# Kernel optimization log

Measured on AMD Instinct MI355X. Metric: run time of the kernel, lower is better.

Reference implementation:

```python
import jax, jax.numpy as jnp
import numpy as np

NUM_HEADS = 16


def setup_inputs() -> dict:
    key = jax.random.key(0)
    ks = jax.random.split(key, 9)
    B, S, D = 2, 2048, 2048
    s = 1.0 / np.sqrt(D)
    return {
        "x": jax.random.normal(ks[0], (B, S, D), jnp.float32),
        "Wq": jax.random.normal(ks[1], (D, D), jnp.float32) * s,
        "bq": jax.random.normal(ks[2], (D,), jnp.float32) * 0.01,
        "Wk": jax.random.normal(ks[3], (D, D), jnp.float32) * s,
        "bk": jax.random.normal(ks[4], (D,), jnp.float32) * 0.01,
        "Wv": jax.random.normal(ks[5], (D, D), jnp.float32) * s,
        "bv": jax.random.normal(ks[6], (D,), jnp.float32) * 0.01,
        "Wo": jax.random.normal(ks[7], (D, D), jnp.float32) * s,
        "bo": jax.random.normal(ks[8], (D,), jnp.float32) * 0.01,
    }


def reference(x, Wq, bq, Wk, bk, Wv, bv, Wo, bo):
    B, S, D = x.shape
    H = NUM_HEADS
    dh = D // H
    # torch Linear: y = x @ W.T + b
    def proj(W, b):
        return (x @ W.T + b).reshape(B, S, H, dh).transpose(0, 2, 1, 3)  # [B,H,S,dh]
    Q = proj(Wq, bq)
    K = proj(Wk, bk)
    V = proj(Wv, bv)
    scores = jnp.einsum('bhqd,bhkd->bhqk', Q, K) / jnp.sqrt(jnp.float32(dh))
    causal = jnp.tril(jnp.ones((S, S), dtype=bool))  # allow k <= q
    scores = jnp.where(causal, scores, -jnp.inf)
    attn = jax.nn.softmax(scores, axis=-1)
    out = jnp.einsum('bhqk,bhkd->bhqd', attn, V)
    out = out.transpose(0, 2, 1, 3).reshape(B, S, D)
    return out @ Wo.T + bo
```

## Files before the change

### kernel.cpp

```cpp
#include <hip/hip_runtime.h>
#include <hip/hip_bf16.h>

#define B_  2
#define S_  2048
#define D_  2048
#define H_  16
#define DH_ 128
#define M_  (B_*S_)

typedef __hip_bfloat16 bf16;
typedef float v4f __attribute__((ext_vector_type(4)));
typedef short v8s __attribute__((ext_vector_type(8)));

__device__ __forceinline__ short f2s(float x) {
  bf16 h = __float2bfloat16(x);
  return *reinterpret_cast<const short*>(&h);
}
__device__ __forceinline__ v8s ld8(const float* p) {
  v4f a = *reinterpret_cast<const v4f*>(p);
  v4f b = *reinterpret_cast<const v4f*>(p + 4);
  v8s r = { f2s(a[0]), f2s(a[1]), f2s(a[2]), f2s(a[3]),
            f2s(b[0]), f2s(b[1]), f2s(b[2]), f2s(b[3]) };
  return r;
}
__device__ __forceinline__ void store_out(bf16* p, float v)  { *p = __float2bfloat16(v); }
__device__ __forceinline__ void store_out(float* p, float v) { *p = v; }

__device__ __forceinline__ void gll16(const bf16* g, bf16* l) {
  __builtin_amdgcn_global_load_lds((const __attribute__((address_space(1))) void*)g,
                                   (__attribute__((address_space(3))) void*)l,
                                   16, 0, 0);
}

__global__ __launch_bounds__(256) void cvt_f32_bf16(const float* __restrict__ in,
                                                    bf16* __restrict__ out, int n8) {
  int i = blockIdx.x * 256 + threadIdx.x;
  if (i >= n8) return;
  *reinterpret_cast<v8s*>(out + (size_t)i * 8) = ld8(in + (size_t)i * 8);
}

__global__ __launch_bounds__(256) void cvt3_f32_bf16(const float* __restrict__ a, bf16* __restrict__ oa,
                                                     const float* __restrict__ b, bf16* __restrict__ ob,
                                                     const float* __restrict__ c, bf16* __restrict__ oc) {
  const int bx = blockIdx.x;
  if (bx < 4096) {
    size_t i = (size_t)bx * 256 + threadIdx.x;
    *reinterpret_cast<v8s*>(oa + i * 8) = ld8(a + i * 8);
  } else if (bx < 6144) {
    size_t i = (size_t)(bx - 4096) * 256 + threadIdx.x;
    *reinterpret_cast<v8s*>(ob + i * 8) = ld8(b + i * 8);
  } else {
    size_t i = (size_t)(bx - 6144) * 256 + threadIdx.x;
    *reinterpret_cast<v8s*>(oc + i * 8) = ld8(c + i * 8);
  }
}

template <int PR>
__device__ __forceinline__ void stage_pair(const bf16* Arow, const bf16* Wrow,
                                           int ktile, bf16* AsD, bf16* BsD,
                                           int tid, int wave) {
  const int k0 = ktile * 64;
#pragma unroll
  for (int u = 0; u < 2; ++u) {
    const int i = PR * 2 + u;
    const int blk = i * 512 + tid;
    if (i < 4) {
      const int row = blk >> 3, c = blk & 7;
      gll16(Arow + (size_t)row * D_ + k0 + ((c ^ (row & 7)) << 3),
            AsD + (i * 512 + wave * 64) * 8);
    } else {
      const int bb = blk - 2048;
      const int row = bb >> 3, c = bb & 7;
      gll16(Wrow + (size_t)row * D_ + k0 + ((c ^ (row & 7)) << 3),
            BsD + ((i - 4) * 512 + wave * 64) * 8);
    }
  }
}

__global__ __launch_bounds__(512, 2) void gemm_qk8(const bf16* __restrict__ A,
                                                   const bf16* __restrict__ W,
                                                   const float* __restrict__ bias0,
                                                   const float* __restrict__ bias1,
                                                   bf16* __restrict__ out0,
                                                   bf16* __restrict__ out1) {
  __shared__ __align__(16) bf16 As0[256 * 64];
  __shared__ __align__(16) bf16 Bs0[256 * 64];
  __shared__ __align__(16) bf16 As1[256 * 64];
  __shared__ __align__(16) bf16 Bs1[256 * 64];
  const int tid  = threadIdx.x;
  const int lane = tid & 63, wave = tid >> 6;
  const int wm = wave >> 2, wn = wave & 3;
  const int quad = lane >> 4, l16 = lane & 15;
  const int swz  = l16 & 7;
  const int bm = blockIdx.y * 256, bn = blockIdx.x * 256;
  const bf16* Arow = A + (size_t)bm * D_;
  const bf16* Wrow = W + (size_t)bn * D_;

  v4f acc[8][4] = {};

  stage_pair<0>(Arow, Wrow, 0, As0, Bs0, tid, wave);
  stage_pair<1>(Arow, Wrow, 0, As0, Bs0, tid, wave);
  stage_pair<2>(Arow, Wrow, 0, As0, Bs0, tid, wave);
  stage_pair<3>(Arow, Wrow, 0, As0, Bs0, tid, wave);

  constexpr int NITER = (D_ / 64) / 2;
  for (int j = 0; j < NITER; ++j) {
    const bool notlast = (j + 1 < NITER);
#pragma unroll
    for (int p = 0; p < 8; ++p) {
      const bf16* Ard = (p < 4) ? As0 : As1;
      const bf16* Brd = (p < 4) ? Bs0 : Bs1;
      bf16* AsD = (p < 4) ? As1 : As0;
      bf16* BsD = (p < 4) ? Bs1 : Bs0;
      const int tstage = (p < 4) ? (2 * j + 1) : (2 * j + 2);

      if (p == 0) {
        stage_pair<0>(Arow, Wrow, tstage, AsD, BsD, tid, wave);
        asm volatile("s_waitcnt vmcnt(2)" ::: "memory");
        __builtin_amdgcn_sched_barrier(0);
        __builtin_amdgcn_s_barrier();
        __builtin_amdgcn_sched_barrier(0);
      } else if (p == 4) {
        if (notlast) {
          stage_pair<0>(Arow, Wrow, tstage, AsD, BsD, tid, wave);
          asm volatile("s_waitcnt vmcnt(2)" ::: "memory");
        } else {
          asm volatile("s_waitcnt vmcnt(0)" ::: "memory");
        }
        __builtin_amdgcn_sched_barrier(0);
        __builtin_amdgcn_s_barrier();
        __builtin_amdgcn_sched_barrier(0);
      } else if (p < 4) {
        if (p == 1) stage_pair<1>(Arow, Wrow, tstage, AsD, BsD, tid, wave);
        if (p == 2) stage_pair<2>(Arow, Wrow, tstage, AsD, BsD, tid, wave);
        if (p == 3) stage_pair<3>(Arow, Wrow, tstage, AsD, BsD, tid, wave);
      } else {
        if (notlast) {
          if (p == 5) stage_pair<1>(Arow, Wrow, tstage, AsD, BsD, tid, wave);
          if (p == 6) stage_pair<2>(Arow, Wrow, tstage, AsD, BsD, tid, wave);
          if (p == 7) stage_pair<3>(Arow, Wrow, tstage, AsD, BsD, tid, wave);
        }
      }

      const int pp = p & 3;
      v8s af[2][2], bfr[4][2];
#pragma unroll
      for (int mi = 0; mi < 2; ++mi)
#pragma unroll
        for (int kk = 0; kk < 2; ++kk) {
          const int row = wm * 128 + (pp * 2 + mi) * 16 + l16;
          af[mi][kk] = *reinterpret_cast<const v8s*>(
              &Ard[row * 64 + (((kk * 4 + quad) ^ swz) << 3)]);
        }
#pragma unroll
      for (int ni = 0; ni < 4; ++ni)
#pragma unroll
        for (int kk = 0; kk < 2; ++kk) {
          const int row = wn * 64 + ni * 16 + l16;
          bfr[ni][kk] = *reinterpret_cast<const v8s*>(
              &Brd[row * 64 + (((kk * 4 + quad) ^ swz) << 3)]);
        }
      __builtin_amdgcn_s_setprio(1);
#pragma unroll
      for (int kk = 0; kk < 2; ++kk)
#pragma unroll
        for (int mi = 0; mi < 2; ++mi)
#pragma unroll
          for (int ni = 0; ni < 4; ++ni)
            acc[pp * 2 + mi][ni] = __builtin_amdgcn_mfma_f32_16x16x32_bf16(
                af[mi][kk], bfr[ni][kk], acc[pp * 2 + mi][ni], 0, 0, 0);
      __builtin_amdgcn_s_setprio(0);
      __builtin_amdgcn_s_barrier();
      __builtin_amdgcn_sched_barrier(0);
    }
  }

  constexpr float QSCALE = 0.12752003912f;
  const int proj = bn >> 11;
  const float* bias = proj ? bias1 : bias0;
  bf16* outp = proj ? out1 : out0;
  const int bnl = bn & 2047;
#pragma unroll
  for (int ni = 0; ni < 4; ++ni) {
    const int nl = bnl + wn * 64 + ni * 16 + l16;
    const float bv = bias[nl];
    const int hh = nl >> 7, d = nl & (DH_ - 1);
#pragma unroll
    for (int mi = 0; mi < 8; ++mi) {
      const int m0 = bm + wm * 128 + mi * 16 + quad * 4;
#pragma unroll
      for (int r = 0; r < 4; ++r) {
        const int m = m0 + r;
        float v = acc[mi][ni][r] + bv;
        if (!proj) v *= QSCALE;
        const int bb = m >> 11, s = m & (S_ - 1);
        outp[((size_t)(bb * H_ + hh) * S_ + s) * DH_ + d] = __float2bfloat16(v);
      }
    }
  }
}

template <int MODE, typename TOUT>
__global__ __launch_bounds__(256) void gemm_bt(const bf16* __restrict__ A,
                                               const bf16* __restrict__ W,
                                               const float* __restrict__ bias0,
                                               TOUT* __restrict__ out0) {
  __shared__ __align__(16) bf16 As[128 * 64];
  __shared__ __align__(16) bf16 Bs[128 * 64];
  const int tid  = threadIdx.x;
  const int lane = tid & 63, wave = tid >> 6;
  const int wm = wave >> 1, wn = wave & 1;
  const int quad = lane >> 4, l16 = lane & 15;
  const int swz  = l16 & 7;
  const int bm = blockIdx.y * 128, bn = blockIdx.x * 128;

  const bf16* Arow = A + (size_t)bm * D_;
  const bf16* Wrow = W + (size_t)bn * D_;

  v4f acc[4][4] = {};
  for (int k0 = 0; k0 < D_; k0 += 64) {
#pragma unroll
    for (int j = 0; j < 4; ++j) {
      const int blk = j * 256 + tid;
      const int row = blk >> 3, c = blk & 7;
      const int gcol = k0 + (((c ^ (row & 7)) << 3));
      gll16(Arow + (size_t)row * D_ + gcol, As + j * 2048 + wave * 512);
      gll16(Wrow + (size_t)row * D_ + gcol, Bs + j * 2048 + wave * 512);
    }
    __syncthreads();
    v8s af[4][2], bfr[4][2];
#pragma unroll
    for (int mi = 0; mi < 4; ++mi)
#pragma unroll
      for (int kk = 0; kk < 2; ++kk)
        af[mi][kk] = *reinterpret_cast<const v8s*>(
            &As[(wm * 64 + mi * 16 + l16) * 64 + (((kk * 4 + quad) ^ swz) << 3)]);
#pragma unroll
    for (int ni = 0; ni < 4; ++ni)
#pragma unroll
      for (int kk = 0; kk < 2; ++kk)
        bfr[ni][kk] = *reinterpret_cast<const v8s*>(
            &Bs[(wn * 64 + ni * 16 + l16) * 64 + (((kk * 4 + quad) ^ swz) << 3)]);
#pragma unroll
    for (int kk = 0; kk < 2; ++kk)
#pragma unroll
      for (int mi = 0; mi < 4; ++mi)
#pragma unroll
        for (int ni = 0; ni < 4; ++ni)
          acc[mi][ni] = __builtin_amdgcn_mfma_f32_16x16x32_bf16(
              af[mi][kk], bfr[ni][kk], acc[mi][ni], 0, 0, 0);
    __syncthreads();
  }

#pragma unroll
  for (int ni = 0; ni < 4; ++ni) {
    const int nl = bn + wn * 64 + ni * 16 + l16;
    const float bv = bias0[nl];
#pragma unroll
    for (int mi = 0; mi < 4; ++mi) {
      const int m0 = bm + wm * 64 + mi * 16 + quad * 4;
#pragma unroll
      for (int r = 0; r < 4; ++r) {
        const int m = m0 + r;
        float v = acc[mi][ni][r] + bv;
        size_t idx;
        if (MODE == 2) {
          int b = m >> 11, s = m & (S_ - 1);
          int h = nl >> 7, d = nl & (DH_ - 1);
          idx = ((size_t)(b * H_ + h) * DH_ + d) * S_ + s;
        } else {
          idx = (size_t)m * D_ + nl;
        }
        store_out(out0 + idx, v);
      }
    }
  }
}

#define QBLK 128
__global__ __launch_bounds__(512, 4) void attn_fused(const bf16* __restrict__ Q,
                                                     const bf16* __restrict__ K,
                                                     const bf16* __restrict__ Vt,
                                                     bf16* __restrict__ Oa) {
  __shared__ __align__(16) bf16 Ks[64 * 128];
  __shared__ __align__(16) bf16 Vs[128 * 64];
  __shared__ __align__(16) bf16 Ps[8][16 * 72];
  const int tid  = threadIdx.x;
  const int lane = tid & 63, wave = tid >> 6;
  const int quad = lane >> 4, l16 = lane & 15;
  const int swz  = l16 & 7;
  const int qtd = (int)gridDim.x - 1 - (int)blockIdx.x;
  const int qt  = (blockIdx.y & 16) ? (int)blockIdx.x : qtd;
  const int bh = blockIdx.y;
  const int b = bh >> 4, h = bh & 15;
  const bf16* Qh = Q  + (size_t)bh * S_ * DH_;
  const bf16* Kh = K  + (size_t)bh * S_ * DH_;
  const bf16* Vh = Vt + (size_t)bh * DH_ * S_;

  const int qrow0 = qt * QBLK + wave * 16;
  v8s qf[4];
#pragma unroll
  for (int kk = 0; kk < 4; ++kk)
    qf[kk] = *reinterpret_cast<const v8s*>(&Qh[(size_t)(qrow0 + l16) * DH_ + kk * 32 + quad * 8]);

  v4f acc_o[8] = {};
  float m_i[4], l_i[4];
#pragma unroll
  for (int r = 0; r < 4; ++r) { m_i[r] = -1.0e30f; l_i[r] = 0.f; }

  const int nkt = 2 * qt + 2;
  for (int kt = 0; kt < nkt; ++kt) {
    const int kbase = kt * 64;
#pragma unroll
    for (int rr = 0; rr < 2; ++rr) {
      const int g = rr * 512 + tid;
      const int krow = g >> 4, kc = g & 15;
      gll16(Kh + (size_t)(kbase + krow) * DH_ + ((kc ^ (krow & 7)) << 3),
            Ks + rr * 4096 + wave * 512);
      const int vrow = g >> 3, vc = g & 7;
      gll16(Vh + (size_t)vrow * S_ + kbase + ((vc ^ (vrow & 7)) << 3),
            Vs + rr * 4096 + wave * 512);
    }
    __syncthreads();

    const bool active = (kbase <= qrow0 + 15);
    if (active) {
      v4f sc[4];
      __builtin_amdgcn_s_setprio(1);
#pragma unroll
      for (int nt = 0; nt < 4; ++nt) {
        v4f a = {};
#pragma unroll
        for (int kk = 0; kk < 4; ++kk) {
          v8s kf = *reinterpret_cast<const v8s*>(
              &Ks[(nt * 16 + l16) * 128 + (((kk * 4 + quad) ^ swz) << 3)]);
          a = __builtin_amdgcn_mfma_f32_16x16x32_bf16(qf[kk], kf, a, 0, 0, 0);
        }
        sc[nt] = a;
      }
      __builtin_amdgcn_s_setprio(0);
      if (kbase + 63 > qrow0) {
#pragma unroll
        for (int nt = 0; nt < 4; ++nt)
#pragma unroll
          for (int r = 0; r < 4; ++r) {
            int kc2 = kbase + nt * 16 + l16;
            int qr = qrow0 + quad * 4 + r;
            if (kc2 > qr) sc[nt][r] = -1.0e30f;
          }
      }
#pragma unroll
      for (int r = 0; r < 4; ++r) {
        float mx = fmaxf(fmaxf(sc[0][r], sc[1][r]), fmaxf(sc[2][r], sc[3][r]));
        mx = fmaxf(mx, __shfl_xor(mx, 1));
        mx = fmaxf(mx, __shfl_xor(mx, 2));
        mx = fmaxf(mx, __shfl_xor(mx, 4));
        mx = fmaxf(mx, __shfl_xor(mx, 8));
        if (mx > m_i[r] + 8.0f) {
          float alpha = exp2f(m_i[r] - mx);
          m_i[r] = mx;
          l_i[r] *= alpha;
#pragma unroll
          for (int nt8 = 0; nt8 < 8; ++nt8) acc_o[nt8][r] *= alpha;
        }
        const float mm = m_i[r];
        float s0 = exp2f(sc[0][r] - mm);
        float s1 = exp2f(sc[1][r] - mm);
        float s2 = exp2f(sc[2][r] - mm);
        float s3 = exp2f(sc[3][r] - mm);
        sc[0][r] = s0; sc[1][r] = s1; sc[2][r] = s2; sc[3][r] = s3;
        float t = s0 + s1 + s2 + s3;
        t += __shfl_xor(t, 1); t += __shfl_xor(t, 2);
        t += __shfl_xor(t, 4); t += __shfl_xor(t, 8);
        l_i[r] += t;
      }
#pragma unroll
      for (int nt = 0; nt < 4; ++nt)
#pragma unroll
        for (int r = 0; r < 4; ++r)
          Ps[wave][(quad * 4 + r) * 72 + nt * 16 + l16] = __float2bfloat16(sc[nt][r]);
      asm volatile("s_waitcnt lgkmcnt(0)" ::: "memory");
      __builtin_amdgcn_s_setprio(1);
#pragma unroll
      for (int kk2 = 0; kk2 < 2; ++kk2) {
        v8s pf = *reinterpret_cast<const v8s*>(&Ps[wave][l16 * 72 + kk2 * 32 + quad * 8]);
#pragma unroll
        for (int nt8 = 0; nt8 < 8; ++nt8) {
          v8s vf = *reinterpret_cast<const v8s*>(
              &Vs[(nt8 * 16 + l16) * 64 + (((kk2 * 4 + quad) ^ swz) << 3)]);
          acc_o[nt8] = __builtin_amdgcn_mfma_f32_16x16x32_bf16(pf, vf, acc_o[nt8], 0, 0, 0);
        }
      }
      __builtin_amdgcn_s_setprio(0);
    }
    __syncthreads();
  }

#pragma unroll
  for (int r = 0; r < 4; ++r) {
    const float inv = 1.0f / l_i[r];
    const int srow = qrow0 + quad * 4 + r;
#pragma unroll
    for (int nt8 = 0; nt8 < 8; ++nt8)
      Oa[((size_t)b * S_ + srow) * D_ + h * DH_ + nt8 * 16 + l16] =
          __float2bfloat16(acc_o[nt8][r] * inv);
  }
}

extern "C" void kernel_launch(void* const* d_in, const int* in_sizes, int n_in,
                              void* d_out, int out_size, void* d_ws, size_t ws_size,
                              hipStream_t stream) {
  if (n_in != 9 ||
      in_sizes[0] != M_ * D_ ||
      in_sizes[1] != D_ * D_ || in_sizes[2] != D_ ||
      in_sizes[3] != D_ * D_ || in_sizes[4] != D_ ||
      in_sizes[5] != D_ * D_ || in_sizes[6] != D_ ||
      in_sizes[7] != D_ * D_ || in_sizes[8] != D_ ||
      out_size != M_ * D_)
    return;

  const float* x  = (const float*)d_in[0];
  const float* Wq = (const float*)d_in[1];
  const float* bq = (const float*)d_in[2];
  const float* Wk = (const float*)d_in[3];
  const float* bk = (const float*)d_in[4];
  const float* Wv = (const float*)d_in[5];
  const float* bv = (const float*)d_in[6];
  const float* Wo = (const float*)d_in[7];
  const float* bo = (const float*)d_in[8];
  float* out = (float*)d_out;

  const size_t NT = (size_t)M_ * D_;
  const size_t WN = (size_t)D_ * D_;
  bf16* qws   = (bf16*)d_out;
  bf16* xbf   = (bf16*)d_out + NT;
  bf16* kws   = (bf16*)d_ws;
  bf16* vtw   = kws + NT;
  bf16* aws   = vtw + NT;
  bf16* wqk   = aws;
  bf16* wv_s  = aws;
  bf16* wo_s  = kws;

  const int N8W = D_ * D_ / 8;

  dim3 bb(256);
  cvt3_f32_bf16<<<8192, bb, 0, stream>>>(x, xbf, Wq, wqk, Wk, wqk + WN);

  gemm_qk8<<<dim3(16, 16), dim3(512), 0, stream>>>(xbf, wqk, bq, bk, qws, kws);

  cvt_f32_bf16<<<N8W / 256, bb, 0, stream>>>(Wv, wv_s, N8W);
  gemm_bt<2, bf16><<<dim3(16, 32), bb, 0, stream>>>(xbf, wv_s, bv, vtw);

  attn_fused<<<dim3(S_ / QBLK, B_ * H_), dim3(512), 0, stream>>>(qws, kws, vtw, aws);

  cvt_f32_bf16<<<N8W / 256, bb, 0, stream>>>(Wo, wo_s, N8W);
  gemm_bt<3, float><<<dim3(16, 32), bb, 0, stream>>>(aws, wo_s, bo, out);
}
```

Baseline: 407.1 us.

## Restructure QK GEMM main loop with register double-buffered A fragments

Rewrites the QK projection GEMM K-loop so each k-tile loads its B fragments once rather than re-reading them for every quarter. A fragments are ping-ponged across two register sets so LDS reads for the next quarter overlap the MFMAs of the current one. Global stages for the next tile are interleaved between MFMA groups, and the per-quarter barriers are replaced by two barriers per k-tile. Intent is to cut LDS traffic and barrier stalls, at the cost of higher register pressure and a different wait/barrier protocol.

```diff
diff --git a/kernel.cpp b/kernel.cpp
--- a/kernel.cpp
+++ b/kernel.cpp
@@ -75,6 +75,68 @@
             BsD + ((i - 4) * 512 + wave * 64) * 8);
     }
   }
+}
+
+#define RD_A(dst, PP)                                                         \
+  _Pragma("unroll")                                                           \
+  for (int mi = 0; mi < 2; ++mi)                                              \
+    _Pragma("unroll")                                                         \
+    for (int kk = 0; kk < 2; ++kk)                                            \
+      dst[mi][kk] = *reinterpret_cast<const v8s*>(                            \
+          &Ard[(wm * 128 + ((PP) * 2 + mi) * 16 + l16) * 64 +                 \
+               (((kk * 4 + quad) ^ swz) << 3)]);
+
+#define MFMA_Q(af, Q)                                                         \
+  __builtin_amdgcn_s_setprio(1);                                              \
+  _Pragma("unroll")                                                           \
+  for (int kk = 0; kk < 2; ++kk)                                              \
+    _Pragma("unroll")                                                         \
+    for (int mi = 0; mi < 2; ++mi)                                            \
+      _Pragma("unroll")                                                       \
+      for (int ni = 0; ni < 4; ++ni)                                          \
+        acc[(Q) * 2 + mi][ni] = __builtin_amdgcn_mfma_f32_16x16x32_bf16(      \
+            af[mi][kk], bfr[ni][kk], acc[(Q) * 2 + mi][ni], 0, 0, 0);         \
+  __builtin_amdgcn_s_setprio(0);
+
+__device__ __forceinline__ void ktile_body(
+    int t, const bf16* Ard, const bf16* Brd,
+    bf16* AsW, bf16* BsW,
+    bf16* AsR, bf16* BsR,
+    const bf16* Arow, const bf16* Wrow,
+    int tid, int wave, int wm, int wn, int quad, int l16, int swz,
+    v4f (&acc)[8][4]) {
+  v8s bfr[4][2];
+#pragma unroll
+  for (int ni = 0; ni < 4; ++ni)
+#pragma unroll
+    for (int kk = 0; kk < 2; ++kk)
+      bfr[ni][kk] = *reinterpret_cast<const v8s*>(
+          &Brd[(wn * 64 + ni * 16 + l16) * 64 + (((kk * 4 + quad) ^ swz) << 3)]);
+  v8s afA[2][2], afB[2][2];
+  RD_A(afA, 0)
+  const bool st = (t + 1 < 32);
+  if (st) stage_pair<1>(Arow, Wrow, t + 1, AsW, BsW, tid, wave);
+  RD_A(afB, 1)
+  MFMA_Q(afA, 0)
+  if (st) stage_pair<2>(Arow, Wrow, t + 1, AsW, BsW, tid, wave);
+  RD_A(afA, 2)
+  MFMA_Q(afB, 1)
+  if (st) stage_pair<3>(Arow, Wrow, t + 1, AsW, BsW, tid, wave);
+  RD_A(afB, 3)
+  MFMA_Q(afA, 2)
+  MFMA_Q(afB, 3)
+  __builtin_amdgcn_sched_barrier(0);
+  __builtin_amdgcn_s_barrier();
+  __builtin_amdgcn_sched_barrier(0);
+  if (t + 2 < 32) {
+    stage_pair<0>(Arow, Wrow, t + 2, AsR, BsR, tid, wave);
+    asm volatile("s_waitcnt vmcnt(2)" ::: "memory");
+  } else {
+    asm volatile("s_waitcnt vmcnt(0)" ::: "memory");
+  }
+  __builtin_amdgcn_sched_barrier(0);
+  __builtin_amdgcn_s_barrier();
+  __builtin_amdgcn_sched_barrier(0);
 }
 
 __global__ __launch_bounds__(512, 2) void gemm_qk8(const bf16* __restrict__ A,
@@ -102,77 +164,17 @@
   stage_pair<1>(Arow, Wrow, 0, As0, Bs0, tid, wave);
   stage_pair<2>(Arow, Wrow, 0, As0, Bs0, tid, wave);
   stage_pair<3>(Arow, Wrow, 0, As0, Bs0, tid, wave);
-
-  constexpr int NITER = (D_ / 64) / 2;
-  for (int j = 0; j < NITER; ++j) {
-    const bool notlast = (j + 1 < NITER);
-#pragma unroll
-    for (int p = 0; p < 8; ++p) {
-      const bf16* Ard = (p < 4) ? As0 : As1;
-      const bf16* Brd = (p < 4) ? Bs0 : Bs1;
-      bf16* AsD = (p < 4) ? As1 : As0;
-      bf16* BsD = (p < 4) ? Bs1 : Bs0;
-      const int tstage = (p < 4) ? (2 * j + 1) : (2 * j + 2);
-
-      if (p == 0) {
-        stage_pair<0>(Arow, Wrow, tstage, AsD, BsD, tid, wave);
-        asm volatile("s_waitcnt vmcnt(2)" ::: "memory");
-        __builtin_amdgcn_sched_barrier(0);
-        __builtin_amdgcn_s_barrier();
-        __builtin_amdgcn_sched_barrier(0);
-      } else if (p == 4) {
-        if (notlast) {
-          stage_pair<0>(Arow, Wrow, tstage, AsD, BsD, tid, wave);
-          asm volatile("s_waitcnt vmcnt(2)" ::: "memory");
-        } else {
-          asm volatile("s_waitcnt vmcnt(0)" ::: "memory");
-        }
-        __builtin_amdgcn_sched_barrier(0);
-        __builtin_amdgcn_s_barrier();
-        __builtin_amdgcn_sched_barrier(0);
-      } else if (p < 4) {
-        if (p == 1) stage_pair<1>(Arow, Wrow, tstage, AsD, BsD, tid, wave);
-        if (p == 2) stage_pair<2>(Arow, Wrow, tstage, AsD, BsD, tid, wave);
-        if (p == 3) stage_pair<3>(Arow, Wrow, tstage, AsD, BsD, tid, wave);
-      } else {
-        if (notlast) {
-          if (p == 5) stage_pair<1>(Arow, Wrow, tstage, AsD, BsD, tid, wave);
-          if (p == 6) stage_pair<2>(Arow, Wrow, tstage, AsD, BsD, tid, wave);
-          if (p == 7) stage_pair<3>(Arow, Wrow, tstage, AsD, BsD, tid, wave);
-        }
-      }
-
-      const int pp = p & 3;
-      v8s af[2][2], bfr[4][2];
-#pragma unroll
-      for (int mi = 0; mi < 2; ++mi)
-#pragma unroll
-        for (int kk = 0; kk < 2; ++kk) {
-          const int row = wm * 128 + (pp * 2 + mi) * 16 + l16;
-          af[mi][kk] = *reinterpret_cast<const v8s*>(
-              &Ard[row * 64 + (((kk * 4 + quad) ^ swz) << 3)]);
-        }
-#pragma unroll
-      for (int ni = 0; ni < 4; ++ni)
-#pragma unroll
-        for (int kk = 0; kk < 2; ++kk) {
-          const int row = wn * 64 + ni * 16 + l16;
-          bfr[ni][kk] = *reinterpret_cast<const v8s*>(
-              &Brd[row * 64 + (((kk * 4 + quad) ^ swz) << 3)]);
-        }
-      __builtin_amdgcn_s_setprio(1);
-#pragma unroll
-      for (int kk = 0; kk < 2; ++kk)
-#pragma unroll
-        for (int mi = 0; mi < 2; ++mi)
-#pragma unroll
-          for (int ni = 0; ni < 4; ++ni)
-            acc[pp * 2 + mi][ni] = __builtin_amdgcn_mfma_f32_16x16x32_bf16(
-                af[mi][kk], bfr[ni][kk], acc[pp * 2 + mi][ni], 0, 0, 0);
-      __builtin_amdgcn_s_setprio(0);
-      __builtin_amdgcn_s_barrier();
-      __builtin_amdgcn_sched_barrier(0);
-    }
+  stage_pair<0>(Arow, Wrow, 1, As1, Bs1, tid, wave);
+  asm volatile("s_waitcnt vmcnt(2)" ::: "memory");
+  __builtin_amdgcn_sched_barrier(0);
+  __builtin_amdgcn_s_barrier();
+  __builtin_amdgcn_sched_barrier(0);
+
+  for (int j = 0; j < 16; ++j) {
+    ktile_body(2 * j,     As0, Bs0, As1, Bs1, As0, Bs0,
+               Arow, Wrow, tid, wave, wm, wn, quad, l16, swz, acc);
+    ktile_body(2 * j + 1, As1, Bs1, As0, Bs0, As1, Bs1,
+               Arow, Wrow, tid, wave, wm, wn, quad, l16, swz, acc);
   }
 
   constexpr float QSCALE = 0.12752003912f;
```

Measured after the change: 401.4 us. Within noise of the previous version (-1.4%).
